# Kernel tuning notes

Hardware: AMD Instinct MI355X
Metric: run time of the kernel (lower is better)

## Reference

```python
import math
import jax, jax.numpy as jnp
import numpy as np

B, N, C = 64, 197, 768
H = 12
D = C // H
SCALE = D ** -0.5
EPS_SM = 1e-6
LN_EPS = 1e-5


def _layernorm(x, w, b):
    mu = jnp.mean(x, axis=-1, keepdims=True)
    var = jnp.var(x, axis=-1, keepdims=True)
    return (x - mu) * jax.lax.rsqrt(var + LN_EPS) * w + b


def setup_inputs() -> dict:
    key = jax.random.key(0)
    ks = jax.random.split(key, 12)
    s = 0.02
    return {
        "x": jax.random.normal(ks[0], (B, N, C), jnp.float32),
        "mask": jnp.ones((B, N), jnp.float32),
        "ln1_w": jnp.ones((C,), jnp.float32),
        "ln1_b": jnp.zeros((C,), jnp.float32),
        "qkv_w": jax.random.normal(ks[1], (C, 3 * C), jnp.float32) * s,
        "qkv_b": jnp.zeros((3 * C,), jnp.float32),
        "proj_w": jax.random.normal(ks[2], (C, C), jnp.float32) * s,
        "proj_b": jnp.zeros((C,), jnp.float32),
        "ln2_w": jnp.ones((C,), jnp.float32),
        "ln2_b": jnp.zeros((C,), jnp.float32),
        "fc1_w": jax.random.normal(ks[3], (C, 4 * C), jnp.float32) * s,
        "fc1_b": jnp.zeros((4 * C,), jnp.float32),
        "fc2_w": jax.random.normal(ks[4], (4 * C, C), jnp.float32) * s,
        "fc2_b": jnp.zeros((C,), jnp.float32),
        "threshold": jnp.float32(0.0),
    }


def reference(x, mask, ln1_w, ln1_b, qkv_w, qkv_b, proj_w, proj_b,
              ln2_w, ln2_b, fc1_w, fc1_b, fc2_w, fc2_b, threshold):
    # --- LTPAttention ---
    h = _layernorm(x, ln1_w, ln1_b)
    qkv = (h @ qkv_w + qkv_b).reshape(B, N, 3, H, D)
    qkv = jnp.transpose(qkv, (2, 0, 3, 1, 4))  # (3, B, H, N, D)
    q, k, v = qkv[0], qkv[1], qkv[2]
    attn = jnp.einsum("bhnd,bhmd->bhnm", q, k) * SCALE  # (B,H,N,N)
    # softmax_with_mask (eval path): exp * key-mask, renormalize
    m = mask[:, None, None, :]  # (B,1,1,N) masks keys
    w = jnp.exp(attn - jnp.max(attn, axis=-1, keepdims=True)) * m
    attn = w / (jnp.sum(w, axis=-1, keepdims=True) + EPS_SM)
    out = jnp.einsum("bhnm,bhmd->bhnd", attn, v)
    out = jnp.transpose(out, (0, 2, 1, 3)).reshape(B, N, C)
    x_attn = out @ proj_w + proj_b
    # importance scores: mean over heads and queries -> (B, N)
    imp = jnp.mean(attn, axis=(1, 2))
    imp = imp.at[:, 0].set(jnp.inf)  # always keep CLS token
    # ThresholdMasker (eval): hard threshold
    new_mask = (imp > threshold).astype(mask.dtype)
    mask_out = jnp.where(mask > 0, new_mask, mask)
    # --- residual + MLP ---
    x = x + x_attn
    h2 = _layernorm(x, ln2_w, ln2_b)
    h2 = jax.nn.gelu(h2 @ fc1_w + fc1_b, approximate=False)
    x = x + (h2 @ fc2_w + fc2_b)
    return x, mask_out
```

## Files before the change

kernel.cpp:

```cpp
#include <hip/hip_runtime.h>
#include <hip/hip_bf16.h>
#include <math.h>

#define B_ 64
#define N_ 197
#define C_ 768
#define H_ 12
#define BN_ (B_ * N_)
#define MPAD 12672
#define GRIDM 99

typedef unsigned short ushort_t;
typedef __attribute__((ext_vector_type(8))) short short8;
typedef __attribute__((ext_vector_type(4))) float f32x4;

__device__ __forceinline__ float wave_reduce_sum(float v) {
#pragma unroll
  for (int off = 32; off; off >>= 1) v += __shfl_xor(v, off);
  return v;
}

__device__ __forceinline__ ushort_t f2bf(float f) {
  __hip_bfloat16 h = __float2bfloat16(f);
  ushort_t u;
  __builtin_memcpy(&u, &h, 2);
  return u;
}

__device__ __forceinline__ float gelu_fast(float u) {
  const float z2 = 1.5957691216f * (u + 0.044715f * u * u * u);
  const float e = __expf(z2);
  const float th = 1.f - 2.f / (e + 1.f);
  return 0.5f * u * (1.f + th);
}

__global__ __launch_bounds__(256) void wtrans_kernel(const float* __restrict__ W,
                                                     ushort_t* __restrict__ Wt,
                                                     int K, int N) {
  __shared__ ushort_t tile[32][33];
  const int bn = blockIdx.x * 32, bk = blockIdx.y * 32;
  const int tx = threadIdx.x & 31, ty = threadIdx.x >> 5;
#pragma unroll
  for (int i = ty; i < 32; i += 8)
    tile[i][tx] = f2bf(W[(size_t)(bk + i) * N + bn + tx]);
  __syncthreads();
#pragma unroll
  for (int i = ty; i < 32; i += 8)
    Wt[(size_t)(bn + i) * K + bk + tx] = tile[tx][i];
}

__global__ __launch_bounds__(256) void ln_kernel(const float* __restrict__ x,
                                                 const float* __restrict__ w,
                                                 const float* __restrict__ bsh,
                                                 ushort_t* __restrict__ out) {
  const int row = blockIdx.x;
  const float* xr = x + (size_t)row * C_;
  const int tid = threadIdx.x;
  float v0 = xr[tid], v1 = xr[tid + 256], v2 = xr[tid + 512];
  float s = v0 + v1 + v2;
  float q = v0 * v0 + v1 * v1 + v2 * v2;
  s = wave_reduce_sum(s);
  q = wave_reduce_sum(q);
  __shared__ float red[8];
  const int w4 = tid >> 6, l = tid & 63;
  if (l == 0) { red[w4] = s; red[4 + w4] = q; }
  __syncthreads();
  float ts = red[0] + red[1] + red[2] + red[3];
  float tq = red[4] + red[5] + red[6] + red[7];
  float mu = ts * (1.f / C_);
  float var = tq * (1.f / C_) - mu * mu;
  float rs = rsqrtf(var + 1e-5f);
  ushort_t* orow = out + (size_t)row * C_;
  orow[tid]       = f2bf((v0 - mu) * rs * w[tid]       + bsh[tid]);
  orow[tid + 256] = f2bf((v1 - mu) * rs * w[tid + 256] + bsh[tid + 256]);
  orow[tid + 512] = f2bf((v2 - mu) * rs * w[tid + 512] + bsh[tid + 512]);
}

template <int RES, int ACT, int OUT_BF16>
__global__ __launch_bounds__(256) void mfma_gemm(const ushort_t* __restrict__ A,
                                                 const ushort_t* __restrict__ Bt,
                                                 const float* __restrict__ bias,
                                                 const float* __restrict__ res,
                                                 void* __restrict__ Cout,
                                                 int M, int Nc, int K, int gridN) {
  __shared__ __align__(16) ushort_t As[2][128][32];
  __shared__ __align__(16) ushort_t Bs[2][128][32];

  const int flat = blockIdx.x;
  const int x8 = flat & 7, q8 = flat >> 3;
  const int n_t = q8 % gridN, jj = q8 / gridN;
  const int m_t = jj * 8 + x8;
  if (m_t >= GRIDM) return;

  const int tid = threadIdx.x;
  const int w = tid >> 6, l = tid & 63;
  const int bm = m_t * 128, bnn = n_t * 128;
  const int quad = l >> 4, lm = l & 15;
  const int wm = (w >> 1) * 64, wn = (w & 1) * 64;

  const int c0 = w * 2, c1 = w * 2 + 1;
  const int srow = l >> 2;
  const int scol = ((l & 3) ^ ((l >> 3) & 3)) << 3;
  const ushort_t* ag0 = A + (size_t)(bm + c0 * 16 + srow) * K + scol;
  const ushort_t* ag1 = A + (size_t)(bm + c1 * 16 + srow) * K + scol;
  const ushort_t* bg0 = Bt + (size_t)(bnn + c0 * 16 + srow) * K + scol;
  const ushort_t* bg1 = Bt + (size_t)(bnn + c1 * 16 + srow) * K + scol;
  ushort_t* la0[2] = {&As[0][c0 * 16][0], &As[1][c0 * 16][0]};
  ushort_t* la1[2] = {&As[0][c1 * 16][0], &As[1][c1 * 16][0]};
  ushort_t* lb0[2] = {&Bs[0][c0 * 16][0], &Bs[1][c0 * 16][0]};
  ushort_t* lb1[2] = {&Bs[0][c1 * 16][0], &Bs[1][c1 * 16][0]};

  auto stage = [&](int pb, int k0) {
    __builtin_amdgcn_global_load_lds(
        (const __attribute__((address_space(1))) void*)(ag0 + k0),
        (__attribute__((address_space(3))) void*)la0[pb], 16, 0, 0);
    __builtin_amdgcn_global_load_lds(
        (const __attribute__((address_space(1))) void*)(ag1 + k0),
        (__attribute__((address_space(3))) void*)la1[pb], 16, 0, 0);
    __builtin_amdgcn_global_load_lds(
        (const __attribute__((address_space(1))) void*)(bg0 + k0),
        (__attribute__((address_space(3))) void*)lb0[pb], 16, 0, 0);
    __builtin_amdgcn_global_load_lds(
        (const __attribute__((address_space(1))) void*)(bg1 + k0),
        (__attribute__((address_space(3))) void*)lb1[pb], 16, 0, 0);
  };

  const int fslot = (quad ^ ((lm >> 1) & 3)) << 3;

  f32x4 acc[4][4];
#pragma unroll
  for (int mi = 0; mi < 4; mi++)
#pragma unroll
    for (int ni = 0; ni < 4; ni++) acc[mi][ni] = (f32x4){0.f, 0.f, 0.f, 0.f};

  const int NIT = K >> 5;
  stage(0, 0);
  int p = 0;
  for (int it = 0; it < NIT; ++it) {
    __syncthreads();
    if (it + 1 < NIT) stage(p ^ 1, (it + 1) << 5);

    short8 af[4], bf[4];
#pragma unroll
    for (int i = 0; i < 4; i++) {
      af[i] = *(const short8*)&As[p][wm + i * 16 + lm][fslot];
      bf[i] = *(const short8*)&Bs[p][wn + i * 16 + lm][fslot];
    }
#pragma unroll
    for (int mi = 0; mi < 4; mi++)
#pragma unroll
      for (int ni = 0; ni < 4; ni++)
        acc[mi][ni] = __builtin_amdgcn_mfma_f32_16x16x32_bf16(
            af[mi], bf[ni], acc[mi][ni], 0, 0, 0);
    p ^= 1;
  }

#pragma unroll
  for (int mi = 0; mi < 4; mi++) {
#pragma unroll
    for (int ni = 0; ni < 4; ni++) {
      const int col = bnn + wn + ni * 16 + lm;
      const float bv = bias[col];
#pragma unroll
      for (int r = 0; r < 4; r++) {
        const int row = bm + wm + mi * 16 + quad * 4 + r;
        if (row < M) {
          float v = acc[mi][ni][r] + bv;
          if constexpr (RES) v += res[(size_t)row * Nc + col];
          if constexpr (ACT) v = gelu_fast(v);
          if constexpr (OUT_BF16)
            ((ushort_t*)Cout)[(size_t)row * Nc + col] = f2bf(v);
          else
            ((float*)Cout)[(size_t)row * Nc + col] = v;
        }
      }
    }
  }
}

__global__ __launch_bounds__(256, 2) void attn_mfma(const ushort_t* __restrict__ qkv,
                                                    const float* __restrict__ mask,
                                                    ushort_t* __restrict__ aout,
                                                    float* __restrict__ imp) {
  __shared__ __align__(16) ushort_t Ks[208 * 64];
  __shared__ __align__(16) ushort_t Vt[64 * 216];
  __shared__ __align__(16) ushort_t Pb[4][16 * 208];
  const int b = blockIdx.x / H_, h = blockIdx.x % H_;
  const int tid = threadIdx.x, w = tid >> 6, l = tid & 63;
  const int quad = l >> 4, lm = l & 15;
  const ushort_t* qbase = qkv + (size_t)b * N_ * 2304 + h * 64;
  const ushort_t* kbase = qbase + 768;
  const ushort_t* vbase = qbase + 1536;

  for (int idx = tid; idx < 208 * 8; idx += 256) {
    const int j = idx >> 3, g = idx & 7;
    uint4 val = make_uint4(0u, 0u, 0u, 0u);
    if (j < N_) val = *(const uint4*)(kbase + (size_t)j * 2304 + g * 8);
    *(uint4*)&Ks[j * 64 + ((g ^ (j & 7)) << 3)] = val;
  }
  for (int idx = tid; idx < 52 * 64; idx += 256) {
    const int d = idx & 63, jg = idx >> 6, j0 = jg * 4;
    ushort_t a0 = 0, a1 = 0, a2 = 0, a3 = 0;
    if (j0 + 0 < N_) a0 = vbase[(size_t)(j0 + 0) * 2304 + d];
    if (j0 + 1 < N_) a1 = vbase[(size_t)(j0 + 1) * 2304 + d];
    if (j0 + 2 < N_) a2 = vbase[(size_t)(j0 + 2) * 2304 + d];
    if (j0 + 3 < N_) a3 = vbase[(size_t)(j0 + 3) * 2304 + d];
    uint2 pk;
    pk.x = (unsigned)a0 | ((unsigned)a1 << 16);
    pk.y = (unsigned)a2 | ((unsigned)a3 << 16);
    *(uint2*)&Vt[d * 216 + j0] = pk;
  }
  float mkv[13];
#pragma unroll
  for (int t = 0; t < 13; t++) {
    const int col = t * 16 + lm;
    mkv[t] = (col < N_) ? mask[b * N_ + col] : 0.f;
  }
  float cs[13];
#pragma unroll
  for (int t = 0; t < 13; t++) cs[t] = 0.f;
  __syncthreads();

  ushort_t* pw = &Pb[w][0];
  for (int i0 = w * 16; i0 < 208; i0 += 64) {
    f32x4 accs[13];
#pragma unroll
    for (int t = 0; t < 13; t++) accs[t] = (f32x4){0.f, 0.f, 0.f, 0.f};
#pragma unroll
    for (int kh = 0; kh < 2; kh++) {
      const int k0 = kh * 32;
      const short8 aq =
          *(const short8*)(qbase + (size_t)(i0 + lm) * 2304 + k0 + quad * 8);
      const int gb = (k0 >> 3) + quad;
#pragma unroll
      for (int t = 0; t < 13; t++) {
        const int j = t * 16 + lm;
        const short8 bk = *(const short8*)&Ks[j * 64 + ((gb ^ (j & 7)) << 3)];
        accs[t] = __builtin_amdgcn_mfma_f32_16x16x32_bf16(aq, bk, accs[t], 0, 0, 0);
      }
    }
    float inv[4];
#pragma unroll
    for (int r = 0; r < 4; r++) {
      float m = -3.4e38f;
#pragma unroll
      for (int t = 0; t < 13; t++) m = fmaxf(m, accs[t][r] * 0.125f);
      m = fmaxf(m, __shfl_xor(m, 1));
      m = fmaxf(m, __shfl_xor(m, 2));
      m = fmaxf(m, __shfl_xor(m, 4));
      m = fmaxf(m, __shfl_xor(m, 8));
      float s = 0.f;
#pragma unroll
      for (int t = 0; t < 13; t++) {
        const float e = __expf(accs[t][r] * 0.125f - m) * mkv[t];
        accs[t][r] = e;
        s += e;
      }
      s += __shfl_xor(s, 1);
      s += __shfl_xor(s, 2);
      s += __shfl_xor(s, 4);
      s += __shfl_xor(s, 8);
      inv[r] = 1.f / (s + 1e-6f);
    }
    const int ibase = i0 + quad * 4;
#pragma unroll
    for (int r = 0; r < 4; r++) {
      const bool rok = (ibase + r) < N_;
#pragma unroll
      for (int t = 0; t < 13; t++) {
        const float p = accs[t][r] * inv[r];
        accs[t][r] = p;
        if (rok) cs[t] += p;
        pw[(quad * 4 + r) * 208 + t * 16 + lm] = f2bf(p);
      }
    }
    __builtin_amdgcn_wave_barrier();
    f32x4 acco[4];
#pragma unroll
    for (int n = 0; n < 4; n++) acco[n] = (f32x4){0.f, 0.f, 0.f, 0.f};
#pragma unroll
    for (int ks = 0; ks < 6; ks++) {
      const int k0 = ks * 32;
      const short8 ap = *(const short8*)&pw[lm * 208 + k0 + quad * 8];
#pragma unroll
      for (int n = 0; n < 4; n++) {
        const short8 bv = *(const short8*)&Vt[(n * 16 + lm) * 216 + k0 + quad * 8];
        acco[n] = __builtin_amdgcn_mfma_f32_16x16x32_bf16(ap, bv, acco[n], 0, 0, 0);
      }
    }
    {
      const bool lo = (quad < 2);
      short8 apt = {};
      if (lo) apt = *(const short8*)&pw[lm * 208 + 192 + quad * 8];
#pragma unroll
      for (int n = 0; n < 4; n++) {
        short8 bvt = {};
        if (lo) bvt = *(const short8*)&Vt[(n * 16 + lm) * 216 + 192 + quad * 8];
        acco[n] = __builtin_amdgcn_mfma_f32_16x16x32_bf16(apt, bvt, acco[n], 0, 0, 0);
      }
    }
#pragma unroll
    for (int r = 0; r < 4; r++) {
      const int i = ibase + r;
      if (i < N_) {
#pragma unroll
        for (int n = 0; n < 4; n++)
          aout[(size_t)(b * N_ + i) * C_ + h * 64 + n * 16 + lm] = f2bf(acco[n][r]);
      }
    }
  }
#pragma unroll
  for (int t = 0; t < 13; t++) {
    float v = cs[t];
    v += __shfl_xor(v, 16);
    v += __shfl_xor(v, 32);
    if (l < 16) {
      const int col = t * 16 + l;
      if (col < N_)
        atomicAdd(&imp[b * N_ + col], v * (1.f / (H_ * (float)N_)));
    }
  }
}

__global__ __launch_bounds__(256) void mask_kernel(const float* __restrict__ imp,
                                                   const float* __restrict__ mask,
                                                   const float* __restrict__ thr,
                                                   float* __restrict__ mask_out) {
  const int i = blockIdx.x * 256 + threadIdx.x;
  if (i >= BN_) return;
  const int n = i % N_;
  const float iv = (n == 0) ? INFINITY : imp[i];
  const float m = mask[i];
  const float nm = (iv > thr[0]) ? 1.f : 0.f;
  mask_out[i] = (m > 0.f) ? nm : m;
}

extern "C" void kernel_launch(void* const* d_in, const int* in_sizes, int n_in,
                              void* d_out, int out_size, void* d_ws, size_t ws_size,
                              hipStream_t stream) {
  const float* x      = (const float*)d_in[0];
  const float* mask   = (const float*)d_in[1];
  const float* ln1_w  = (const float*)d_in[2];
  const float* ln1_b  = (const float*)d_in[3];
  const float* qkv_w  = (const float*)d_in[4];
  const float* qkv_b  = (const float*)d_in[5];
  const float* proj_w = (const float*)d_in[6];
  const float* proj_b = (const float*)d_in[7];
  const float* ln2_w  = (const float*)d_in[8];
  const float* ln2_b  = (const float*)d_in[9];
  const float* fc1_w  = (const float*)d_in[10];
  const float* fc1_b  = (const float*)d_in[11];
  const float* fc2_w  = (const float*)d_in[12];
  const float* fc2_b  = (const float*)d_in[13];
  const float* thr    = (const float*)d_in[14];

  float* out = (float*)d_out;
  float* mask_out = out + (size_t)BN_ * C_;

  ushort_t* buf0    = (ushort_t*)d_ws;
  ushort_t* hbuf    = buf0 + (size_t)MPAD * 3072;
  ushort_t* aoutb   = hbuf + (size_t)MPAD * 768;
  ushort_t* qkv_wt  = aoutb + (size_t)MPAD * 768;
  ushort_t* proj_wt = qkv_wt + (size_t)2304 * 768;
  ushort_t* fc1_wt  = proj_wt + (size_t)768 * 768;
  ushort_t* fc2_wt  = fc1_wt + (size_t)3072 * 768;
  float*    impb    = (float*)(fc2_wt + (size_t)768 * 3072);

  hipMemsetAsync(impb, 0, BN_ * sizeof(float), stream);

  wtrans_kernel<<<dim3(2304 / 32, 768 / 32), 256, 0, stream>>>(qkv_w, qkv_wt, 768, 2304);
  wtrans_kernel<<<dim3(768 / 32, 768 / 32), 256, 0, stream>>>(proj_w, proj_wt, 768, 768);
  wtrans_kernel<<<dim3(3072 / 32, 768 / 32), 256, 0, stream>>>(fc1_w, fc1_wt, 768, 3072);
  wtrans_kernel<<<dim3(768 / 32, 3072 / 32), 256, 0, stream>>>(fc2_w, fc2_wt, 3072, 768);

  const int MS = 13 * 8;
  ln_kernel<<<BN_, 256, 0, stream>>>(x, ln1_w, ln1_b, hbuf);
  mfma_gemm<0, 0, 1><<<MS * 18, 256, 0, stream>>>(
      hbuf, qkv_wt, qkv_b, nullptr, buf0, BN_, 2304, 768, 18);
  attn_mfma<<<B_ * H_, 256, 0, stream>>>(buf0, mask, aoutb, impb);
  mask_kernel<<<(BN_ + 255) / 256, 256, 0, stream>>>(impb, mask, thr, mask_out);
  mfma_gemm<1, 0, 0><<<MS * 6, 256, 0, stream>>>(
      aoutb, proj_wt, proj_b, x, out, BN_, 768, 768, 6);
  ln_kernel<<<BN_, 256, 0, stream>>>(out, ln2_w, ln2_b, hbuf);
  mfma_gemm<0, 1, 1><<<MS * 24, 256, 0, stream>>>(
      hbuf, fc1_wt, fc1_b, nullptr, buf0, BN_, 3072, 768, 24);
  mfma_gemm<1, 0, 0><<<MS * 6, 256, 0, stream>>>(
      buf0, fc2_wt, fc2_b, out, out, BN_, 768, 3072, 6);
}
```

Baseline: 572.6 us.

## Enlarge GEMM tiles to 256-row blocks with 4-stage LDS pipeline

Replaces the 128x128 double-buffered MFMA GEMM with a 512-thread kernel using 256-row tiles (256x256 for QKV/FC1, 256x128 for proj/FC2). Staging is now a 4-slot ring with three tiles in flight, gated by explicit vmcnt waits and a raw barrier instead of __syncthreads. The aim is more operand reuse per LDS byte and better hiding of global-load latency. In exchange it uses more LDS and registers (launch bounds 512,2), launches fewer blocks, and clamps out-of-range A rows to row 0.

```diff
diff --git a/kernel.cpp b/kernel.cpp
--- a/kernel.cpp
+++ b/kernel.cpp
@@ -8,7 +8,6 @@
 #define H_ 12
 #define BN_ (B_ * N_)
 #define MPAD 12672
-#define GRIDM 99
 
 typedef unsigned short ushort_t;
 typedef __attribute__((ext_vector_type(8))) short short8;
@@ -76,89 +75,105 @@
   orow[tid + 512] = f2bf((v2 - mu) * rs * w[tid + 512] + bsh[tid + 512]);
 }
 
-template <int RES, int ACT, int OUT_BF16>
-__global__ __launch_bounds__(256) void mfma_gemm(const ushort_t* __restrict__ A,
-                                                 const ushort_t* __restrict__ Bt,
-                                                 const float* __restrict__ bias,
-                                                 const float* __restrict__ res,
-                                                 void* __restrict__ Cout,
-                                                 int M, int Nc, int K, int gridN) {
-  __shared__ __align__(16) ushort_t As[2][128][32];
-  __shared__ __align__(16) ushort_t Bs[2][128][32];
+template <int BN_T, int RES, int ACT, int OUT_BF16>
+__global__ __launch_bounds__(512, 2) void mfma_gemm2(const ushort_t* __restrict__ A,
+                                                     const ushort_t* __restrict__ Bt,
+                                                     const float* __restrict__ bias,
+                                                     const float* __restrict__ res,
+                                                     void* __restrict__ Cout,
+                                                     int M, int Nc, int K, int gridN) {
+  __shared__ __align__(16) ushort_t As[4][256][32];
+  __shared__ __align__(16) ushort_t Bs[4][BN_T][32];
 
   const int flat = blockIdx.x;
   const int x8 = flat & 7, q8 = flat >> 3;
   const int n_t = q8 % gridN, jj = q8 / gridN;
   const int m_t = jj * 8 + x8;
-  if (m_t >= GRIDM) return;
+  const int gridM = (M + 255) >> 8;
+  if (m_t >= gridM) return;
 
   const int tid = threadIdx.x;
   const int w = tid >> 6, l = tid & 63;
-  const int bm = m_t * 128, bnn = n_t * 128;
   const int quad = l >> 4, lm = l & 15;
-  const int wm = (w >> 1) * 64, wn = (w & 1) * 64;
-
-  const int c0 = w * 2, c1 = w * 2 + 1;
+  const int bm = m_t * 256, bnn = n_t * BN_T;
+
+  constexpr int MR = (BN_T == 256) ? 8 : 4;
+  constexpr int NR = 4;
+  constexpr int LPI = (BN_T == 256) ? 4 : 3;
+  constexpr int VMC = 2 * LPI;
+  const int wm = (BN_T == 256) ? (w >> 2) * 128 : (w >> 1) * 64;
+  const int wn = (BN_T == 256) ? (w & 3) * 64 : (w & 1) * 64;
+
   const int srow = l >> 2;
   const int scol = ((l & 3) ^ ((l >> 3) & 3)) << 3;
-  const ushort_t* ag0 = A + (size_t)(bm + c0 * 16 + srow) * K + scol;
-  const ushort_t* ag1 = A + (size_t)(bm + c1 * 16 + srow) * K + scol;
-  const ushort_t* bg0 = Bt + (size_t)(bnn + c0 * 16 + srow) * K + scol;
-  const ushort_t* bg1 = Bt + (size_t)(bnn + c1 * 16 + srow) * K + scol;
-  ushort_t* la0[2] = {&As[0][c0 * 16][0], &As[1][c0 * 16][0]};
-  ushort_t* la1[2] = {&As[0][c1 * 16][0], &As[1][c1 * 16][0]};
-  ushort_t* lb0[2] = {&Bs[0][c0 * 16][0], &Bs[1][c0 * 16][0]};
-  ushort_t* lb1[2] = {&Bs[0][c1 * 16][0], &Bs[1][c1 * 16][0]};
-
-  auto stage = [&](int pb, int k0) {
+  int ar0 = bm + w * 32 + srow;      if (ar0 >= MPAD) ar0 = 0;
+  int ar1 = bm + w * 32 + 16 + srow; if (ar1 >= MPAD) ar1 = 0;
+  const ushort_t* ag0 = A + (size_t)ar0 * K + scol;
+  const ushort_t* ag1 = A + (size_t)ar1 * K + scol;
+  const int brow0 = bnn + ((BN_T == 256) ? w * 32 : w * 16) + srow;
+  const ushort_t* bg0 = Bt + (size_t)brow0 * K + scol;
+  const ushort_t* bg1 = Bt + (size_t)(bnn + w * 32 + 16 + srow) * K + scol;
+
+  auto stage = [&](int slot, int tile) {
+    const int k0 = tile << 5;
     __builtin_amdgcn_global_load_lds(
         (const __attribute__((address_space(1))) void*)(ag0 + k0),
-        (__attribute__((address_space(3))) void*)la0[pb], 16, 0, 0);
+        (__attribute__((address_space(3))) void*)&As[slot][w * 32][0], 16, 0, 0);
     __builtin_amdgcn_global_load_lds(
         (const __attribute__((address_space(1))) void*)(ag1 + k0),
-        (__attribute__((address_space(3))) void*)la1[pb], 16, 0, 0);
-    __builtin_amdgcn_global_load_lds(
-        (const __attribute__((address_space(1))) void*)(bg0 + k0),
-        (__attribute__((address_space(3))) void*)lb0[pb], 16, 0, 0);
-    __builtin_amdgcn_global_load_lds(
-        (const __attribute__((address_space(1))) void*)(bg1 + k0),
-        (__attribute__((address_space(3))) void*)lb1[pb], 16, 0, 0);
+        (__attribute__((address_space(3))) void*)&As[slot][w * 32 + 16][0], 16, 0, 0);
+    if constexpr (BN_T == 256) {
+      __builtin_amdgcn_global_load_lds(
+          (const __attribute__((address_space(1))) void*)(bg0 + k0),
+          (__attribute__((address_space(3))) void*)&Bs[slot][w * 32][0], 16, 0, 0);
+      __builtin_amdgcn_global_load_lds(
+          (const __attribute__((address_space(1))) void*)(bg1 + k0),
+          (__attribute__((address_space(3))) void*)&Bs[slot][w * 32 + 16][0], 16, 0, 0);
+    } else {
+      __builtin_amdgcn_global_load_lds(
+          (const __attribute__((address_space(1))) void*)(bg0 + k0),
+          (__attribute__((address_space(3))) void*)&Bs[slot][w * 16][0], 16, 0, 0);
+    }
   };
 
   const int fslot = (quad ^ ((lm >> 1) & 3)) << 3;
 
-  f32x4 acc[4][4];
-#pragma unroll
-  for (int mi = 0; mi < 4; mi++)
-#pragma unroll
-    for (int ni = 0; ni < 4; ni++) acc[mi][ni] = (f32x4){0.f, 0.f, 0.f, 0.f};
+  f32x4 acc[MR][NR];
+#pragma unroll
+  for (int mi = 0; mi < MR; mi++)
+#pragma unroll
+    for (int ni = 0; ni < NR; ni++) acc[mi][ni] = (f32x4){0.f, 0.f, 0.f, 0.f};
 
   const int NIT = K >> 5;
   stage(0, 0);
-  int p = 0;
+  stage(1, 1);
+  stage(2, 2);
   for (int it = 0; it < NIT; ++it) {
-    __syncthreads();
-    if (it + 1 < NIT) stage(p ^ 1, (it + 1) << 5);
-
-    short8 af[4], bf[4];
-#pragma unroll
-    for (int i = 0; i < 4; i++) {
-      af[i] = *(const short8*)&As[p][wm + i * 16 + lm][fslot];
-      bf[i] = *(const short8*)&Bs[p][wn + i * 16 + lm][fslot];
-    }
-#pragma unroll
-    for (int mi = 0; mi < 4; mi++)
-#pragma unroll
-      for (int ni = 0; ni < 4; ni++)
-        acc[mi][ni] = __builtin_amdgcn_mfma_f32_16x16x32_bf16(
-            af[mi], bf[ni], acc[mi][ni], 0, 0, 0);
-    p ^= 1;
-  }
-
-#pragma unroll
-  for (int mi = 0; mi < 4; mi++) {
-#pragma unroll
-    for (int ni = 0; ni < 4; ni++) {
+    const int slot = it & 3;
+    asm volatile("s_waitcnt vmcnt(%0)" ::"n"(VMC) : "memory");
+    __builtin_amdgcn_s_barrier();
+    asm volatile("" ::: "memory");
+    if (it + 3 < NIT) stage((it + 3) & 3, it + 3);
+
+    short8 af[MR], bfr[NR];
+#pragma unroll
+    for (int i = 0; i < MR; i++)
+      af[i] = *(const short8*)&As[slot][wm + i * 16 + lm][fslot];
+#pragma unroll
+    for (int n = 0; n < NR; n++)
+      bfr[n] = *(const short8*)&Bs[slot][wn + n * 16 + lm][fslot];
+#pragma unroll
+    for (int mi = 0; mi < MR; mi++)
+#pragma unroll
+      for (int ni = 0; ni < NR; ni++)
+        acc[mi][ni] = __builtin_amdgcn_mfma_f32_16x16x32_bf16(af[mi], bfr[ni],
+                                                              acc[mi][ni], 0, 0, 0);
+  }
+
+#pragma unroll
+  for (int mi = 0; mi < MR; mi++) {
+#pragma unroll
+    for (int ni = 0; ni < NR; ni++) {
       const int col = bnn + wn + ni * 16 + lm;
       const float bv = bias[col];
 #pragma unroll
@@ -373,17 +388,18 @@
   wtrans_kernel<<<dim3(3072 / 32, 768 / 32), 256, 0, stream>>>(fc1_w, fc1_wt, 768, 3072);
   wtrans_kernel<<<dim3(768 / 32, 3072 / 32), 256, 0, stream>>>(fc2_w, fc2_wt, 3072, 768);
 
-  const int MS = 13 * 8;
+  const int MS2 = 56;
+
   ln_kernel<<<BN_, 256, 0, stream>>>(x, ln1_w, ln1_b, hbuf);
-  mfma_gemm<0, 0, 1><<<MS * 18, 256, 0, stream>>>(
-      hbuf, qkv_wt, qkv_b, nullptr, buf0, BN_, 2304, 768, 18);
+  mfma_gemm2<256, 0, 0, 1><<<MS2 * 9, 512, 0, stream>>>(
+      hbuf, qkv_wt, qkv_b, nullptr, buf0, BN_, 2304, 768, 9);
   attn_mfma<<<B_ * H_, 256, 0, stream>>>(buf0, mask, aoutb, impb);
   mask_kernel<<<(BN_ + 255) / 256, 256, 0, stream>>>(impb, mask, thr, mask_out);
-  mfma_gemm<1, 0, 0><<<MS * 6, 256, 0, stream>>>(
+  mfma_gemm2<128, 1, 0, 0><<<MS2 * 6, 512, 0, stream>>>(
       aoutb, proj_wt, proj_b, x, out, BN_, 768, 768, 6);
   ln_kernel<<<BN_, 256, 0, stream>>>(out, ln2_w, ln2_b, hbuf);
-  mfma_gemm<0, 1, 1><<<MS * 24, 256, 0, stream>>>(
-      hbuf, fc1_wt, fc1_b, nullptr, buf0, BN_, 3072, 768, 24);
-  mfma_gemm<1, 0, 0><<<MS * 6, 256, 0, stream>>>(
+  mfma_gemm2<256, 0, 1, 1><<<MS2 * 12, 512, 0, stream>>>(
+      hbuf, fc1_wt, fc1_b, nullptr, buf0, BN_, 3072, 768, 12);
+  mfma_gemm2<128, 1, 0, 0><<<MS2 * 6, 512, 0, stream>>>(
       buf0, fc2_wt, fc2_b, out, out, BN_, 768, 3072, 6);
 }
```

Result: slower. 722.5 us (+26.2%).

## Deepen GEMM LDS pipeline to four stages with explicit vmcnt waits

Applied to the files above, without the earlier changes.

Replaces the double-buffered LDS staging in the MFMA GEMM with a four-buffer ring that keeps three k-tiles of global_load_lds in flight. It waits with explicit s_waitcnt vmcnt counts plus a raw barrier instead of __syncthreads, so global loads overlap more MFMA work. In exchange the kernel uses twice the LDS, which may cut occupancy. The loop also assumes K/32 is a multiple of 4 and at least 4.

```diff
diff --git a/kernel.cpp b/kernel.cpp
--- a/kernel.cpp
+++ b/kernel.cpp
@@ -83,8 +83,14 @@
                                                  const float* __restrict__ res,
                                                  void* __restrict__ Cout,
                                                  int M, int Nc, int K, int gridN) {
-  __shared__ __align__(16) ushort_t As[2][128][32];
-  __shared__ __align__(16) ushort_t Bs[2][128][32];
+  __shared__ __align__(16) ushort_t As0[128][32];
+  __shared__ __align__(16) ushort_t As1[128][32];
+  __shared__ __align__(16) ushort_t As2[128][32];
+  __shared__ __align__(16) ushort_t As3[128][32];
+  __shared__ __align__(16) ushort_t Bs0[128][32];
+  __shared__ __align__(16) ushort_t Bs1[128][32];
+  __shared__ __align__(16) ushort_t Bs2[128][32];
+  __shared__ __align__(16) ushort_t Bs3[128][32];
 
   const int flat = blockIdx.x;
   const int x8 = flat & 7, q8 = flat >> 3;
@@ -105,24 +111,20 @@
   const ushort_t* ag1 = A + (size_t)(bm + c1 * 16 + srow) * K + scol;
   const ushort_t* bg0 = Bt + (size_t)(bnn + c0 * 16 + srow) * K + scol;
   const ushort_t* bg1 = Bt + (size_t)(bnn + c1 * 16 + srow) * K + scol;
-  ushort_t* la0[2] = {&As[0][c0 * 16][0], &As[1][c0 * 16][0]};
-  ushort_t* la1[2] = {&As[0][c1 * 16][0], &As[1][c1 * 16][0]};
-  ushort_t* lb0[2] = {&Bs[0][c0 * 16][0], &Bs[1][c0 * 16][0]};
-  ushort_t* lb1[2] = {&Bs[0][c1 * 16][0], &Bs[1][c1 * 16][0]};
-
-  auto stage = [&](int pb, int k0) {
+
+  auto stage = [&](ushort_t (*Ad)[32], ushort_t (*Bd)[32], int k0) {
     __builtin_amdgcn_global_load_lds(
         (const __attribute__((address_space(1))) void*)(ag0 + k0),
-        (__attribute__((address_space(3))) void*)la0[pb], 16, 0, 0);
+        (__attribute__((address_space(3))) void*)&Ad[c0 * 16][0], 16, 0, 0);
     __builtin_amdgcn_global_load_lds(
         (const __attribute__((address_space(1))) void*)(ag1 + k0),
-        (__attribute__((address_space(3))) void*)la1[pb], 16, 0, 0);
+        (__attribute__((address_space(3))) void*)&Ad[c1 * 16][0], 16, 0, 0);
     __builtin_amdgcn_global_load_lds(
         (const __attribute__((address_space(1))) void*)(bg0 + k0),
-        (__attribute__((address_space(3))) void*)lb0[pb], 16, 0, 0);
+        (__attribute__((address_space(3))) void*)&Bd[c0 * 16][0], 16, 0, 0);
     __builtin_amdgcn_global_load_lds(
         (const __attribute__((address_space(1))) void*)(bg1 + k0),
-        (__attribute__((address_space(3))) void*)lb1[pb], 16, 0, 0);
+        (__attribute__((address_space(3))) void*)&Bd[c1 * 16][0], 16, 0, 0);
   };
 
   const int fslot = (quad ^ ((lm >> 1) & 3)) << 3;
@@ -134,26 +136,39 @@
     for (int ni = 0; ni < 4; ni++) acc[mi][ni] = (f32x4){0.f, 0.f, 0.f, 0.f};
 
   const int NIT = K >> 5;
-  stage(0, 0);
-  int p = 0;
-  for (int it = 0; it < NIT; ++it) {
-    __syncthreads();
-    if (it + 1 < NIT) stage(p ^ 1, (it + 1) << 5);
-
-    short8 af[4], bf[4];
-#pragma unroll
-    for (int i = 0; i < 4; i++) {
-      af[i] = *(const short8*)&As[p][wm + i * 16 + lm][fslot];
-      bf[i] = *(const short8*)&Bs[p][wn + i * 16 + lm][fslot];
-    }
-#pragma unroll
-    for (int mi = 0; mi < 4; mi++)
-#pragma unroll
-      for (int ni = 0; ni < 4; ni++)
-        acc[mi][ni] = __builtin_amdgcn_mfma_f32_16x16x32_bf16(
-            af[mi], bf[ni], acc[mi][ni], 0, 0, 0);
-    p ^= 1;
-  }
+
+#define GSTEP(Ac, Bc, An, Bn, tn, VMN, DOSTAGE)                         \
+  {                                                                     \
+    asm volatile("s_waitcnt vmcnt(" #VMN ")" ::: "memory");             \
+    __builtin_amdgcn_s_barrier();                                       \
+    asm volatile("" ::: "memory");                                      \
+    if (DOSTAGE) stage(An, Bn, (tn) << 5);                              \
+    short8 af[4], bf[4];                                                \
+    _Pragma("unroll") for (int i = 0; i < 4; i++) {                     \
+      af[i] = *(const short8*)&Ac[wm + i * 16 + lm][fslot];             \
+      bf[i] = *(const short8*)&Bc[wn + i * 16 + lm][fslot];             \
+    }                                                                   \
+    _Pragma("unroll") for (int mi = 0; mi < 4; mi++)                    \
+      _Pragma("unroll") for (int ni = 0; ni < 4; ni++)                  \
+        acc[mi][ni] = __builtin_amdgcn_mfma_f32_16x16x32_bf16(          \
+            af[mi], bf[ni], acc[mi][ni], 0, 0, 0);                      \
+  }
+
+  stage(As0, Bs0, 0);
+  stage(As1, Bs1, 1 << 5);
+  stage(As2, Bs2, 2 << 5);
+  int t = 0;
+  for (; t < NIT - 4; t += 4) {
+    GSTEP(As0, Bs0, As3, Bs3, t + 3, 8, true);
+    GSTEP(As1, Bs1, As0, Bs0, t + 4, 8, true);
+    GSTEP(As2, Bs2, As1, Bs1, t + 5, 8, true);
+    GSTEP(As3, Bs3, As2, Bs2, t + 6, 8, true);
+  }
+  GSTEP(As0, Bs0, As3, Bs3, t + 3, 8, true);
+  GSTEP(As1, Bs1, As0, Bs0, 0, 8, false);
+  GSTEP(As2, Bs2, As0, Bs0, 0, 4, false);
+  GSTEP(As3, Bs3, As0, Bs0, 0, 0, false);
+#undef GSTEP
 
 #pragma unroll
   for (int mi = 0; mi < 4; mi++) {
```

Result: slower. 603.3 us (+5.4%).

## Switch GEMM to single-wave 64x64 tiles with barrier-free vmcnt pipelining

Applied to the files above, without the earlier changes.

Replaces the 256-thread 128x128-tile GEMM with a 64-thread single-wave kernel computing 64x64 tiles. Because only one wave touches the LDS tile, __syncthreads is replaced by explicit s_waitcnt vmcnt double buffering in an unrolled loop. M=12608 divides evenly by 64, so row bounds checks and the padded workspace are dropped. This removes the tile-quantization waste and block-wide barriers, at the cost of less data reuse per tile and more global/L2 traffic.

```diff
diff --git a/kernel.cpp b/kernel.cpp
--- a/kernel.cpp
+++ b/kernel.cpp
@@ -7,8 +7,7 @@
 #define C_ 768
 #define H_ 12
 #define BN_ (B_ * N_)
-#define MPAD 12672
-#define GRIDM 99
+#define GRIDM64 197
 
 typedef unsigned short ushort_t;
 typedef __attribute__((ext_vector_type(8))) short short8;
@@ -77,52 +76,52 @@
 }
 
 template <int RES, int ACT, int OUT_BF16>
-__global__ __launch_bounds__(256) void mfma_gemm(const ushort_t* __restrict__ A,
-                                                 const ushort_t* __restrict__ Bt,
-                                                 const float* __restrict__ bias,
-                                                 const float* __restrict__ res,
-                                                 void* __restrict__ Cout,
-                                                 int M, int Nc, int K, int gridN) {
-  __shared__ __align__(16) ushort_t As[2][128][32];
-  __shared__ __align__(16) ushort_t Bs[2][128][32];
+__global__ __launch_bounds__(64) void mfma_gemm(const ushort_t* __restrict__ A,
+                                                const ushort_t* __restrict__ Bt,
+                                                const float* __restrict__ bias,
+                                                const float* __restrict__ res,
+                                                void* __restrict__ Cout,
+                                                int M, int Nc, int K, int gridN) {
+  __shared__ __align__(16) ushort_t As0[64][32];
+  __shared__ __align__(16) ushort_t As1[64][32];
+  __shared__ __align__(16) ushort_t Bs0[64][32];
+  __shared__ __align__(16) ushort_t Bs1[64][32];
 
   const int flat = blockIdx.x;
   const int x8 = flat & 7, q8 = flat >> 3;
   const int n_t = q8 % gridN, jj = q8 / gridN;
   const int m_t = jj * 8 + x8;
-  if (m_t >= GRIDM) return;
-
-  const int tid = threadIdx.x;
-  const int w = tid >> 6, l = tid & 63;
-  const int bm = m_t * 128, bnn = n_t * 128;
+  if (m_t >= GRIDM64) return;
+
+  const int l = threadIdx.x;
   const int quad = l >> 4, lm = l & 15;
-  const int wm = (w >> 1) * 64, wn = (w & 1) * 64;
-
-  const int c0 = w * 2, c1 = w * 2 + 1;
+  const int bm = m_t * 64, bnn = n_t * 64;
+
   const int srow = l >> 2;
   const int scol = ((l & 3) ^ ((l >> 3) & 3)) << 3;
-  const ushort_t* ag0 = A + (size_t)(bm + c0 * 16 + srow) * K + scol;
-  const ushort_t* ag1 = A + (size_t)(bm + c1 * 16 + srow) * K + scol;
-  const ushort_t* bg0 = Bt + (size_t)(bnn + c0 * 16 + srow) * K + scol;
-  const ushort_t* bg1 = Bt + (size_t)(bnn + c1 * 16 + srow) * K + scol;
-  ushort_t* la0[2] = {&As[0][c0 * 16][0], &As[1][c0 * 16][0]};
-  ushort_t* la1[2] = {&As[0][c1 * 16][0], &As[1][c1 * 16][0]};
-  ushort_t* lb0[2] = {&Bs[0][c0 * 16][0], &Bs[1][c0 * 16][0]};
-  ushort_t* lb1[2] = {&Bs[0][c1 * 16][0], &Bs[1][c1 * 16][0]};
-
-  auto stage = [&](int pb, int k0) {
-    __builtin_amdgcn_global_load_lds(
-        (const __attribute__((address_space(1))) void*)(ag0 + k0),
-        (__attribute__((address_space(3))) void*)la0[pb], 16, 0, 0);
-    __builtin_amdgcn_global_load_lds(
-        (const __attribute__((address_space(1))) void*)(ag1 + k0),
-        (__attribute__((address_space(3))) void*)la1[pb], 16, 0, 0);
-    __builtin_amdgcn_global_load_lds(
-        (const __attribute__((address_space(1))) void*)(bg0 + k0),
-        (__attribute__((address_space(3))) void*)lb0[pb], 16, 0, 0);
-    __builtin_amdgcn_global_load_lds(
-        (const __attribute__((address_space(1))) void*)(bg1 + k0),
-        (__attribute__((address_space(3))) void*)lb1[pb], 16, 0, 0);
+  const ushort_t* ap[4];
+  const ushort_t* bp[4];
+#pragma unroll
+  for (int i = 0; i < 4; i++) {
+    ap[i] = A + (size_t)(bm + i * 16 + srow) * K + scol;
+    bp[i] = Bt + (size_t)(bnn + i * 16 + srow) * K + scol;
+  }
+
+  auto stage = [&](ushort_t (*Ad)[32], ushort_t (*Bd)[32]) {
+#pragma unroll
+    for (int i = 0; i < 4; i++) {
+      __builtin_amdgcn_global_load_lds(
+          (const __attribute__((address_space(1))) void*)ap[i],
+          (__attribute__((address_space(3))) void*)&Ad[i * 16][0], 16, 0, 0);
+      ap[i] += 32;
+    }
+#pragma unroll
+    for (int i = 0; i < 4; i++) {
+      __builtin_amdgcn_global_load_lds(
+          (const __attribute__((address_space(1))) void*)bp[i],
+          (__attribute__((address_space(3))) void*)&Bd[i * 16][0], 16, 0, 0);
+      bp[i] += 32;
+    }
   };
 
   const int fslot = (quad ^ ((lm >> 1) & 3)) << 3;
@@ -134,45 +133,49 @@
     for (int ni = 0; ni < 4; ni++) acc[mi][ni] = (f32x4){0.f, 0.f, 0.f, 0.f};
 
   const int NIT = K >> 5;
-  stage(0, 0);
-  int p = 0;
-  for (int it = 0; it < NIT; ++it) {
-    __syncthreads();
-    if (it + 1 < NIT) stage(p ^ 1, (it + 1) << 5);
-
-    short8 af[4], bf[4];
-#pragma unroll
-    for (int i = 0; i < 4; i++) {
-      af[i] = *(const short8*)&As[p][wm + i * 16 + lm][fslot];
-      bf[i] = *(const short8*)&Bs[p][wn + i * 16 + lm][fslot];
-    }
-#pragma unroll
-    for (int mi = 0; mi < 4; mi++)
-#pragma unroll
-      for (int ni = 0; ni < 4; ni++)
-        acc[mi][ni] = __builtin_amdgcn_mfma_f32_16x16x32_bf16(
-            af[mi], bf[ni], acc[mi][ni], 0, 0, 0);
-    p ^= 1;
-  }
+
+#define GSTEP(Ac, Bc, An, Bn, VMN, DOSTAGE)                              \
+  {                                                                      \
+    if (DOSTAGE) stage(An, Bn);                                          \
+    asm volatile("s_waitcnt vmcnt(" #VMN ")" ::: "memory");              \
+    __builtin_amdgcn_sched_barrier(0);                                   \
+    short8 af[4], bf[4];                                                 \
+    _Pragma("unroll") for (int i = 0; i < 4; i++) {                      \
+      af[i] = *(const short8*)&Ac[i * 16 + lm][fslot];                   \
+      bf[i] = *(const short8*)&Bc[i * 16 + lm][fslot];                   \
+    }                                                                    \
+    _Pragma("unroll") for (int mi = 0; mi < 4; mi++)                     \
+      _Pragma("unroll") for (int ni = 0; ni < 4; ni++)                   \
+        acc[mi][ni] = __builtin_amdgcn_mfma_f32_16x16x32_bf16(           \
+            af[mi], bf[ni], acc[mi][ni], 0, 0, 0);                       \
+  }
+
+  stage(As0, Bs0);
+  int t = 0;
+  for (; t + 2 < NIT; t += 2) {
+    GSTEP(As0, Bs0, As1, Bs1, 8, 1);
+    GSTEP(As1, Bs1, As0, Bs0, 8, 1);
+  }
+  GSTEP(As0, Bs0, As1, Bs1, 8, 1);
+  GSTEP(As1, Bs1, As0, Bs0, 0, 0);
+#undef GSTEP
 
 #pragma unroll
   for (int mi = 0; mi < 4; mi++) {
 #pragma unroll
     for (int ni = 0; ni < 4; ni++) {
-      const int col = bnn + wn + ni * 16 + lm;
+      const int col = bnn + ni * 16 + lm;
       const float bv = bias[col];
 #pragma unroll
       for (int r = 0; r < 4; r++) {
-        const int row = bm + wm + mi * 16 + quad * 4 + r;
-        if (row < M) {
-          float v = acc[mi][ni][r] + bv;
-          if constexpr (RES) v += res[(size_t)row * Nc + col];
-          if constexpr (ACT) v = gelu_fast(v);
-          if constexpr (OUT_BF16)
-            ((ushort_t*)Cout)[(size_t)row * Nc + col] = f2bf(v);
-          else
-            ((float*)Cout)[(size_t)row * Nc + col] = v;
-        }
+        const int row = bm + mi * 16 + quad * 4 + r;
+        float v = acc[mi][ni][r] + bv;
+        if constexpr (RES) v += res[(size_t)row * Nc + col];
+        if constexpr (ACT) v = gelu_fast(v);
+        if constexpr (OUT_BF16)
+          ((ushort_t*)Cout)[(size_t)row * Nc + col] = f2bf(v);
+        else
+          ((float*)Cout)[(size_t)row * Nc + col] = v;
       }
     }
   }
@@ -358,9 +361,9 @@
   float* mask_out = out + (size_t)BN_ * C_;
 
   ushort_t* buf0    = (ushort_t*)d_ws;
-  ushort_t* hbuf    = buf0 + (size_t)MPAD * 3072;
-  ushort_t* aoutb   = hbuf + (size_t)MPAD * 768;
-  ushort_t* qkv_wt  = aoutb + (size_t)MPAD * 768;
+  ushort_t* hbuf    = buf0 + (size_t)BN_ * 3072;
+  ushort_t* aoutb   = hbuf + (size_t)BN_ * 768;
+  ushort_t* qkv_wt  = aoutb + (size_t)BN_ * 768;
   ushort_t* proj_wt = qkv_wt + (size_t)2304 * 768;
   ushort_t* fc1_wt  = proj_wt + (size_t)768 * 768;
   ushort_t* fc2_wt  = fc1_wt + (size_t)3072 * 768;
@@ -373,17 +376,17 @@
   wtrans_kernel<<<dim3(3072 / 32, 768 / 32), 256, 0, stream>>>(fc1_w, fc1_wt, 768, 3072);
   wtrans_kernel<<<dim3(768 / 32, 3072 / 32), 256, 0, stream>>>(fc2_w, fc2_wt, 3072, 768);
 
-  const int MS = 13 * 8;
+  const int MS = 25 * 8;
   ln_kernel<<<BN_, 256, 0, stream>>>(x, ln1_w, ln1_b, hbuf);
-  mfma_gemm<0, 0, 1><<<MS * 18, 256, 0, stream>>>(
-      hbuf, qkv_wt, qkv_b, nullptr, buf0, BN_, 2304, 768, 18);
+  mfma_gemm<0, 0, 1><<<MS * 36, 64, 0, stream>>>(
+      hbuf, qkv_wt, qkv_b, nullptr, buf0, BN_, 2304, 768, 36);
   attn_mfma<<<B_ * H_, 256, 0, stream>>>(buf0, mask, aoutb, impb);
   mask_kernel<<<(BN_ + 255) / 256, 256, 0, stream>>>(impb, mask, thr, mask_out);
-  mfma_gemm<1, 0, 0><<<MS * 6, 256, 0, stream>>>(
-      aoutb, proj_wt, proj_b, x, out, BN_, 768, 768, 6);
+  mfma_gemm<1, 0, 0><<<MS * 12, 64, 0, stream>>>(
+      aoutb, proj_wt, proj_b, x, out, BN_, 768, 768, 12);
   ln_kernel<<<BN_, 256, 0, stream>>>(out, ln2_w, ln2_b, hbuf);
-  mfma_gemm<0, 1, 1><<<MS * 24, 256, 0, stream>>>(
-      hbuf, fc1_wt, fc1_b, nullptr, buf0, BN_, 3072, 768, 24);
-  mfma_gemm<1, 0, 0><<<MS * 6, 256, 0, stream>>>(
-      buf0, fc2_wt, fc2_b, out, out, BN_, 768, 3072, 6);
-}
+  mfma_gemm<0, 1, 1><<<MS * 48, 64, 0, stream>>>(
+      hbuf, fc1_wt, fc1_b, nullptr, buf0, BN_, 3072, 768, 48);
+  mfma_gemm<1, 0, 0><<<MS * 12, 64, 0, stream>>>(
+      buf0, fc2_wt, fc2_b, out, out, BN_, 768, 3072, 12);
+}
```

Result: slower. 651.8 us (+13.8%).
